# Optimization experiments

Measured on AMD Instinct MI355X. Metric: run time of the kernel, lower is better.

Reference implementation:

```python
import jax, jax.numpy as jnp
import numpy as np

N_NODES = 100000
N_EDGES = 1600000
NFEAT = 256
NHID = 64
NHEADS = 8
NCLASS = 97
ALPHA = 0.2  # leaky relu slope
EPS = 1e-16  # guard against isolated rows (pyGAT divides by e_rowsum directly)


def _sp_gat_layer(x, Wk, ak, src, dst, n_nodes, alpha, concat):
    """One SpGraphAttentionLayer (eval mode, dropout off).
    x: [N, f_in], Wk: [f_in, f_out], ak: [2*f_out].
    edge e_ij = exp(-leakyrelu(a . [h_i || h_j])), out[i] = sum_j e_ij h_j / sum_j e_ij.
    """
    h = x @ Wk                          # [N, f_out]
    f_out = Wk.shape[1]
    s_src = h @ ak[:f_out]              # [N] = a1 . h_i
    s_dst = h @ ak[f_out:]              # [N] = a2 . h_j
    e = jnp.exp(-jax.nn.leaky_relu(s_src[src] + s_dst[dst], negative_slope=alpha))  # [E]
    rowsum = jax.ops.segment_sum(e, src, num_segments=n_nodes)                       # [N]
    num = jax.ops.segment_sum(e[:, None] * h[dst], src, num_segments=n_nodes)        # [N, f_out]
    h_prime = num / (rowsum[:, None] + EPS)
    return jax.nn.elu(h_prime) if concat else h_prime


def setup_inputs() -> dict:
    key = jax.random.key(0)
    ks = jax.random.split(key, 6)
    gain = 1.414  # xavier gain used by pyGAT
    features = jax.random.normal(ks[0], (N_NODES, NFEAT), dtype=jnp.float32)
    edge_index = jax.random.randint(ks[1], (2, N_EDGES), 0, N_NODES, dtype=jnp.int64)
    W = jax.random.normal(ks[2], (NHEADS, NFEAT, NHID), dtype=jnp.float32) * (gain * np.sqrt(2.0 / (NFEAT + NHID)))
    a = jax.random.normal(ks[3], (NHEADS, 2 * NHID), dtype=jnp.float32) * (gain * np.sqrt(2.0 / (1 + 2 * NHID)))
    W_out = jax.random.normal(ks[4], (NHEADS * NHID, NCLASS), dtype=jnp.float32) * (gain * np.sqrt(2.0 / (NHEADS * NHID + NCLASS)))
    a_out = jax.random.normal(ks[5], (2 * NCLASS,), dtype=jnp.float32) * (gain * np.sqrt(2.0 / (1 + 2 * NCLASS)))
    return {"features": features, "W": W, "a": a, "W_out": W_out, "a_out": a_out, "edge_index": edge_index}


def reference(features, W, a, W_out, a_out, edge_index):
    src, dst = edge_index[0], edge_index[1]
    n = features.shape[0]
    # multi-head hidden layer, concat heads (loop over small fixed head count to bound memory)
    heads = [
        _sp_gat_layer(features, W[k], a[k], src, dst, n, ALPHA, concat=True)
        for k in range(W.shape[0])
    ]
    x = jnp.concatenate(heads, axis=1)  # [N, nheads*nhid]
    # output attention layer (concat=False), then elu + log_softmax as in SpGAT.forward
    x = _sp_gat_layer(x, W_out, a_out, src, dst, n, ALPHA, concat=False)
    return jax.nn.log_softmax(jax.nn.elu(x), axis=1)
```

## Files before the change

kernel.cpp:

```cpp
#include <hip/hip_runtime.h>
#include <hip/hip_bf16.h>
#include <stdint.h>

typedef __attribute__((ext_vector_type(8))) short short8;
typedef __attribute__((ext_vector_type(4))) float floatx4;
typedef uint32_t u32;

#define N_NODES 100000
#define N_EDGES 1600000
#define ALPHA_SLOPE 0.2f
#define EPS_F 1e-16f

static __device__ __forceinline__ float bf2f(ushort h) {
    u32 u = ((u32)h) << 16;
    return __builtin_bit_cast(float, u);
}
static __device__ __forceinline__ ushort f2bf(float f) {
    u32 u = __builtin_bit_cast(u32, f);
    u32 r = (u + 0x7fffu + ((u >> 16) & 1u)) >> 16;
    return (ushort)r;
}
static __device__ __forceinline__ float edge_e(float s) {
    float lr = s > 0.f ? s : ALPHA_SLOPE * s;
    return __expf(-lr);
}

__global__ __launch_bounds__(256) void prep(
    const float* __restrict__ feat, const float* __restrict__ W,
    const float* __restrict__ Wout, const float* __restrict__ a,
    const float* __restrict__ aout, const int* __restrict__ ei,
    ushort* __restrict__ featb, ushort* __restrict__ Bp1, ushort* __restrict__ Bp2,
    float* __restrict__ acol1, float* __restrict__ acol2, int* __restrict__ cnt)
{
    int b = blockIdx.x;
    if (b < 25000) {
        int i = b * 256 + threadIdx.x;
        float4 v = ((const float4*)feat)[i];
        ushort4 o;
        o.x = f2bf(v.x); o.y = f2bf(v.y); o.z = f2bf(v.z); o.w = f2bf(v.w);
        ((ushort4*)featb)[i] = o;
    } else if (b < 25512) {
        int idx = (b - 25000) * 256 + threadIdx.x;
        if (idx < 256 * 512) {
            int k = idx >> 9, n = idx & 511;
            int head = n >> 6, c = n & 63;
            Bp1[((size_t)(k >> 3) * 512 + n) * 8 + (k & 7)] = f2bf(W[head * 16384 + k * 64 + c]);
        }
        if (idx < 512 * 128) {
            int k = idx >> 7, n = idx & 127;
            ushort v = (n < 97) ? f2bf(Wout[k * 97 + n]) : (ushort)0;
            Bp2[((size_t)(k >> 3) * 128 + n) * 8 + (k & 7)] = v;
        }
        if (idx < 512) {
            int head = idx >> 6, c = idx & 63;
            acol1[idx * 2]     = a[head * 128 + c];
            acol1[idx * 2 + 1] = a[head * 128 + 64 + c];
        }
        if (idx < 128) {
            acol2[idx * 2]     = (idx < 97) ? aout[idx] : 0.f;
            acol2[idx * 2 + 1] = (idx < 97) ? aout[97 + idx] : 0.f;
        }
    } else {
        int e = (b - 25512) * 256 + threadIdx.x;
        atomicAdd(&cnt[ei[e]], 1);
    }
}

__global__ __launch_bounds__(256) void gemm_mfma(
    const ushort* __restrict__ A, const ushort* __restrict__ Bp,
    ushort* __restrict__ C, const float* __restrict__ acol,
    float* __restrict__ ssrc_arr, float* __restrict__ sdst_arr,
    int sstride, int M, int K, int NP)
{
    __shared__ __align__(16) ushort Ald[8 * 128 * 8];
    const int tid = threadIdx.x;
    const int lane = tid & 63;
    const int wave = tid >> 6;
    const int wr = wave >> 1, wc = wave & 1;
    const int row0 = blockIdx.y * 128;
    const int col0 = blockIdx.x * 128;
    const int quad = lane >> 4;
    const int l16 = lane & 15;

    floatx4 acc[4][4] = {};

    for (int k0 = 0; k0 < K; k0 += 64) {
        __syncthreads();
#pragma unroll
        for (int i = 0; i < 4; ++i) {
            int q = i * 256 + tid;
            int r = q >> 3, kq = q & 7;
            int row = row0 + r;
            if (row >= M) row = M - 1;
            const uint4* src = (const uint4*)(A + (size_t)row * K + k0 + kq * 8);
            *(uint4*)(&Ald[(kq * 128 + (r ^ kq)) * 8]) = *src;
        }
        __syncthreads();

#pragma unroll
        for (int s = 0; s < 2; ++s) {
            int kqq = s * 4 + quad;
            int kqg = (k0 >> 3) + kqq;
            short8 bfrag[4];
#pragma unroll
            for (int nt = 0; nt < 4; ++nt) {
                int col = col0 + wc * 64 + nt * 16 + l16;
                bfrag[nt] = *(const short8*)(Bp + ((size_t)kqg * NP + col) * 8);
            }
#pragma unroll
            for (int mt = 0; mt < 4; ++mt) {
                int r = wr * 64 + mt * 16 + l16;
                short8 afrag = *(const short8*)(&Ald[(kqq * 128 + (r ^ kqq)) * 8]);
#pragma unroll
                for (int nt = 0; nt < 4; ++nt) {
                    acc[mt][nt] = __builtin_amdgcn_mfma_f32_16x16x32_bf16(afrag, bfrag[nt], acc[mt][nt], 0, 0, 0);
                }
            }
        }
    }

#pragma unroll
    for (int mt = 0; mt < 4; ++mt) {
#pragma unroll
        for (int rr = 0; rr < 4; ++rr) {
            int row = row0 + wr * 64 + mt * 16 + quad * 4 + rr;
            if (row < M) {
#pragma unroll
                for (int nt = 0; nt < 4; ++nt) {
                    int col = col0 + wc * 64 + nt * 16 + l16;
                    C[(size_t)row * NP + col] = f2bf(acc[mt][nt][rr]);
                }
            }
        }
    }

    float av1[4], av2[4];
#pragma unroll
    for (int nt = 0; nt < 4; ++nt) {
        int col = col0 + wc * 64 + nt * 16 + l16;
        av1[nt] = acol[col * 2];
        av2[nt] = acol[col * 2 + 1];
    }
    int g = (col0 + wc * 64) >> 6;
    int goff = (sstride > 1) ? g : 0;
#pragma unroll
    for (int mt = 0; mt < 4; ++mt) {
#pragma unroll
        for (int rr = 0; rr < 4; ++rr) {
            float p1 = 0.f, p2 = 0.f;
#pragma unroll
            for (int nt = 0; nt < 4; ++nt) {
                p1 = fmaf(acc[mt][nt][rr], av1[nt], p1);
                p2 = fmaf(acc[mt][nt][rr], av2[nt], p2);
            }
#pragma unroll
            for (int o = 1; o < 16; o <<= 1) {
                p1 += __shfl_xor(p1, o);
                p2 += __shfl_xor(p2, o);
            }
            int row = row0 + wr * 64 + mt * 16 + quad * 4 + rr;
            if (l16 == 0 && row < M) {
                atomicAdd(&ssrc_arr[(size_t)row * sstride + goff], p1);
                atomicAdd(&sdst_arr[(size_t)row * sstride + goff], p2);
            }
        }
    }
}

__global__ __launch_bounds__(256) void scan_partial(const int* __restrict__ cnt, int* __restrict__ bsum, int N) {
    int idx = blockIdx.x * 256 + threadIdx.x;
    int v = (idx < N) ? cnt[idx] : 0;
#pragma unroll
    for (int o = 32; o; o >>= 1) v += __shfl_xor(v, o);
    __shared__ int ws[4];
    if ((threadIdx.x & 63) == 0) ws[threadIdx.x >> 6] = v;
    __syncthreads();
    if (threadIdx.x == 0) bsum[blockIdx.x] = ws[0] + ws[1] + ws[2] + ws[3];
}

__global__ __launch_bounds__(512) void scan_block(int* __restrict__ bsum, int nb) {
    __shared__ int s[512];
    int t = threadIdx.x;
    int v = (t < nb) ? bsum[t] : 0;
    s[t] = v;
    __syncthreads();
    for (int o = 1; o < 512; o <<= 1) {
        int u = (t >= o) ? s[t - o] : 0;
        __syncthreads();
        s[t] += u;
        __syncthreads();
    }
    if (t < nb) bsum[t] = s[t] - v;
}

__global__ __launch_bounds__(256) void scan_final(
    const int* __restrict__ cnt, const int* __restrict__ bsum,
    int* __restrict__ row_ptr, int N, int E)
{
    int b = blockIdx.x, t = threadIdx.x;
    int idx = b * 256 + t;
    int v = (idx < N) ? cnt[idx] : 0;
    __shared__ int s[256];
    s[t] = v;
    __syncthreads();
    for (int o = 1; o < 256; o <<= 1) {
        int u = (t >= o) ? s[t - o] : 0;
        __syncthreads();
        s[t] += u;
        __syncthreads();
    }
    if (idx < N) row_ptr[idx] = bsum[b] + s[t] - v;
    if (idx == 0) row_ptr[N] = E;
}

__global__ __launch_bounds__(256) void fill_csr(
    const int* __restrict__ ei, const int* __restrict__ row_ptr,
    int* __restrict__ cur, int* __restrict__ col_idx, int E)
{
    int e = blockIdx.x * 256 + threadIdx.x;
    if (e >= E) return;
    int s = ei[e];
    int d = ei[E + e];
    int p = atomicAdd(&cur[s], 1);
    col_idx[row_ptr[s] + p] = d;
}

__global__ __launch_bounds__(256) void ea1(
    const int* __restrict__ row_ptr, const int* __restrict__ col_idx,
    const ushort* __restrict__ h_all, const float* __restrict__ ssrc1,
    const float* __restrict__ sdst1, ushort* __restrict__ x1)
{
    int w = blockIdx.x * 4 + (threadIdx.x >> 6);
    int l = threadIdx.x & 63;
    int hl = l >> 3;
    int start = row_ptr[w], end = row_ptr[w + 1];
    float si = ssrc1[(size_t)w * 8 + hl];
    float acc[8] = {};
    float re = 0.f;
    int j = start;
    for (; j + 4 <= end; j += 4) {
        int d0 = col_idx[j], d1 = col_idx[j + 1], d2 = col_idx[j + 2], d3 = col_idx[j + 3];
        float e0 = edge_e(si + sdst1[(size_t)d0 * 8 + hl]);
        float e1 = edge_e(si + sdst1[(size_t)d1 * 8 + hl]);
        float e2 = edge_e(si + sdst1[(size_t)d2 * 8 + hl]);
        float e3 = edge_e(si + sdst1[(size_t)d3 * 8 + hl]);
        short8 v0 = *(const short8*)(h_all + (size_t)d0 * 512 + l * 8);
        short8 v1 = *(const short8*)(h_all + (size_t)d1 * 512 + l * 8);
        short8 v2 = *(const short8*)(h_all + (size_t)d2 * 512 + l * 8);
        short8 v3 = *(const short8*)(h_all + (size_t)d3 * 512 + l * 8);
        re += (e0 + e1) + (e2 + e3);
#pragma unroll
        for (int q = 0; q < 8; ++q) {
            float t0 = fmaf(e0, bf2f((ushort)v0[q]), e1 * bf2f((ushort)v1[q]));
            float t1 = fmaf(e2, bf2f((ushort)v2[q]), e3 * bf2f((ushort)v3[q]));
            acc[q] += t0 + t1;
        }
    }
    for (; j < end; ++j) {
        int d = col_idx[j];
        float e = edge_e(si + sdst1[(size_t)d * 8 + hl]);
        short8 hv = *(const short8*)(h_all + (size_t)d * 512 + l * 8);
        re += e;
#pragma unroll
        for (int q = 0; q < 8; ++q)
            acc[q] = fmaf(e, bf2f((ushort)hv[q]), acc[q]);
    }
    float inv = 1.f / (re + EPS_F);
    short8 o;
#pragma unroll
    for (int q = 0; q < 8; ++q) {
        float p = acc[q] * inv;
        p = p > 0.f ? p : expm1f(p);
        o[q] = (short)f2bf(p);
    }
    __builtin_nontemporal_store(o, (short8*)(x1 + (size_t)w * 512 + l * 8));
}

__global__ __launch_bounds__(256) void ea2(
    const int* __restrict__ row_ptr, const int* __restrict__ col_idx,
    const ushort* __restrict__ h2p, const float* __restrict__ s2src,
    const float* __restrict__ s2dst, float* __restrict__ out)
{
    int w = blockIdx.x * 8 + (threadIdx.x >> 5);
    int l = threadIdx.x & 31;
    int start = row_ptr[w], end = row_ptr[w + 1];
    float si = s2src[w];
    float a0 = 0.f, a1 = 0.f, a2 = 0.f, a3 = 0.f, re = 0.f;
    int j = start;
    for (; j + 4 <= end; j += 4) {
        int d0 = col_idx[j], d1 = col_idx[j + 1], d2 = col_idx[j + 2], d3 = col_idx[j + 3];
        float e0 = edge_e(si + s2dst[d0]);
        float e1 = edge_e(si + s2dst[d1]);
        float e2 = edge_e(si + s2dst[d2]);
        float e3 = edge_e(si + s2dst[d3]);
        ushort4 h0 = *(const ushort4*)(h2p + (size_t)d0 * 128 + 4 * l);
        ushort4 h1 = *(const ushort4*)(h2p + (size_t)d1 * 128 + 4 * l);
        ushort4 h2 = *(const ushort4*)(h2p + (size_t)d2 * 128 + 4 * l);
        ushort4 h3 = *(const ushort4*)(h2p + (size_t)d3 * 128 + 4 * l);
        re += (e0 + e1) + (e2 + e3);
        a0 += fmaf(e0, bf2f(h0.x), e1 * bf2f(h1.x)) + fmaf(e2, bf2f(h2.x), e3 * bf2f(h3.x));
        a1 += fmaf(e0, bf2f(h0.y), e1 * bf2f(h1.y)) + fmaf(e2, bf2f(h2.y), e3 * bf2f(h3.y));
        a2 += fmaf(e0, bf2f(h0.z), e1 * bf2f(h1.z)) + fmaf(e2, bf2f(h2.z), e3 * bf2f(h3.z));
        a3 += fmaf(e0, bf2f(h0.w), e1 * bf2f(h1.w)) + fmaf(e2, bf2f(h2.w), e3 * bf2f(h3.w));
    }
    for (; j < end; ++j) {
        int d = col_idx[j];
        float e = edge_e(si + s2dst[d]);
        ushort4 hv = *(const ushort4*)(h2p + (size_t)d * 128 + 4 * l);
        re += e;
        a0 = fmaf(e, bf2f(hv.x), a0);
        a1 = fmaf(e, bf2f(hv.y), a1);
        a2 = fmaf(e, bf2f(hv.z), a2);
        a3 = fmaf(e, bf2f(hv.w), a3);
    }
    float inv = 1.f / (re + EPS_F);
    float v[4] = { a0 * inv, a1 * inv, a2 * inv, a3 * inv };
    bool val[4];
    float m = -1e30f;
#pragma unroll
    for (int q = 0; q < 4; ++q) {
        v[q] = v[q] > 0.f ? v[q] : expm1f(v[q]);
        val[q] = (4 * l + q) < 97;
        if (val[q]) m = fmaxf(m, v[q]);
    }
#pragma unroll
    for (int o = 16; o; o >>= 1) m = fmaxf(m, __shfl_xor(m, o));
    float ex = 0.f;
#pragma unroll
    for (int q = 0; q < 4; ++q) ex += val[q] ? __expf(v[q] - m) : 0.f;
#pragma unroll
    for (int o = 16; o; o >>= 1) ex += __shfl_xor(ex, o);
    float lt = m + logf(ex);
#pragma unroll
    for (int q = 0; q < 4; ++q)
        if (val[q]) __builtin_nontemporal_store(v[q] - lt, out + (size_t)w * 97 + 4 * l + q);
}

extern "C" void kernel_launch(void* const* d_in, const int* in_sizes, int n_in,
                              void* d_out, int out_size, void* d_ws, size_t ws_size,
                              hipStream_t stream)
{
    const float* feat = (const float*)d_in[0];
    const float* W    = (const float*)d_in[1];
    const float* a    = (const float*)d_in[2];
    const float* Wout = (const float*)d_in[3];
    const float* aout = (const float*)d_in[4];
    const int*   ei   = (const int*)d_in[5];
    float* out = (float*)d_out;

    const int N = N_NODES, E = N_EDGES;
    const int NB = (N + 255) / 256;

    char* base = (char*)d_ws;
    ushort* h_all = (ushort*)(base);
    ushort* x1    = (ushort*)(base + 102400000);
    ushort* featb = (ushort*)(base + 204800000);
    ushort* h2p   = (ushort*)(base + 204800000);
    char* tail = base + 256000000;
    float* ssrc1   = (float*)(tail + 0);
    float* sdst1   = (float*)(tail + 3200000);
    float* s2src   = (float*)(tail + 6400000);
    float* s2dst   = (float*)(tail + 6800000);
    int*   row_ptr = (int*)(tail + 7200000);
    int*   cnt     = (int*)(tail + 7600128);
    int*   cur     = (int*)(tail + 8000128);
    int*   col_idx = (int*)(tail + 8400128);
    int*   bsum    = (int*)(tail + 14800128);
    ushort* Bp1    = (ushort*)(tail + 14801920);
    ushort* Bp2    = (ushort*)(tail + 15064064);
    float* acol1   = (float*)(tail + 15195136);
    float* acol2   = (float*)(tail + 15199232);

    hipMemsetAsync(ssrc1, 0, (size_t)8400128, stream);

    prep<<<31762, 256, 0, stream>>>(feat, W, Wout, a, aout, ei, featb, Bp1, Bp2, acol1, acol2, cnt);

    gemm_mfma<<<dim3(4, 782), 256, 0, stream>>>(featb, Bp1, h_all, acol1, ssrc1, sdst1, 8, N, 256, 512);

    scan_partial<<<NB, 256, 0, stream>>>(cnt, bsum, N);
    scan_block<<<1, 512, 0, stream>>>(bsum, NB);
    scan_final<<<NB, 256, 0, stream>>>(cnt, bsum, row_ptr, N, E);
    fill_csr<<<(E + 255) / 256, 256, 0, stream>>>(ei, row_ptr, cur, col_idx, E);

    ea1<<<N / 4, 256, 0, stream>>>(row_ptr, col_idx, h_all, ssrc1, sdst1, x1);

    gemm_mfma<<<dim3(1, 782), 256, 0, stream>>>(x1, Bp2, h2p, acol2, s2src, s2dst, 1, N, 512, 128);
    ea2<<<N / 8, 256, 0, stream>>>(row_ptr, col_idx, h2p, s2src, s2dst, out);
}
```

Baseline: 823.2 us.

## Fuse layer-1 attention aggregation with layer-2 projection GEMM via LDS tile

After: 774.5 us. 5.9% less time.

```diff
diff --git a/kernel.cpp b/kernel.cpp
--- a/kernel.cpp
+++ b/kernel.cpp
@@ -225,55 +225,112 @@
     col_idx[row_ptr[s] + p] = d;
 }
 
-__global__ __launch_bounds__(256) void ea1(
+__global__ __launch_bounds__(256, 6) void ea1p(
     const int* __restrict__ row_ptr, const int* __restrict__ col_idx,
     const ushort* __restrict__ h_all, const float* __restrict__ ssrc1,
-    const float* __restrict__ sdst1, ushort* __restrict__ x1)
-{
-    int w = blockIdx.x * 4 + (threadIdx.x >> 6);
-    int l = threadIdx.x & 63;
-    int hl = l >> 3;
-    int start = row_ptr[w], end = row_ptr[w + 1];
-    float si = ssrc1[(size_t)w * 8 + hl];
-    float acc[8] = {};
-    float re = 0.f;
-    int j = start;
-    for (; j + 4 <= end; j += 4) {
-        int d0 = col_idx[j], d1 = col_idx[j + 1], d2 = col_idx[j + 2], d3 = col_idx[j + 3];
-        float e0 = edge_e(si + sdst1[(size_t)d0 * 8 + hl]);
-        float e1 = edge_e(si + sdst1[(size_t)d1 * 8 + hl]);
-        float e2 = edge_e(si + sdst1[(size_t)d2 * 8 + hl]);
-        float e3 = edge_e(si + sdst1[(size_t)d3 * 8 + hl]);
-        short8 v0 = *(const short8*)(h_all + (size_t)d0 * 512 + l * 8);
-        short8 v1 = *(const short8*)(h_all + (size_t)d1 * 512 + l * 8);
-        short8 v2 = *(const short8*)(h_all + (size_t)d2 * 512 + l * 8);
-        short8 v3 = *(const short8*)(h_all + (size_t)d3 * 512 + l * 8);
-        re += (e0 + e1) + (e2 + e3);
+    const float* __restrict__ sdst1, const ushort* __restrict__ Bp2,
+    const float* __restrict__ acol2, ushort* __restrict__ h2p,
+    float* __restrict__ s2src, float* __restrict__ s2dst)
+{
+    __shared__ __align__(16) ushort Xs[16 * 512];
+    const int tid = threadIdx.x;
+    const int l = tid & 63;
+    const int wv = tid >> 6;
+    const int hl = l >> 3;
+    const int blk = blockIdx.x;
+
+#pragma unroll 1
+    for (int i = 0; i < 4; ++i) {
+        int r = wv * 4 + i;
+        int node = __builtin_amdgcn_readfirstlane(blk * 16 + r);
+        int start = row_ptr[node], end = row_ptr[node + 1];
+        float si = ssrc1[(size_t)node * 8 + hl];
+        float acc[8] = {};
+        float re = 0.f;
+        int j = start;
+        for (; j + 4 <= end; j += 4) {
+            int d0 = col_idx[j], d1 = col_idx[j + 1], d2 = col_idx[j + 2], d3 = col_idx[j + 3];
+            float e0 = edge_e(si + sdst1[(size_t)d0 * 8 + hl]);
+            float e1 = edge_e(si + sdst1[(size_t)d1 * 8 + hl]);
+            float e2 = edge_e(si + sdst1[(size_t)d2 * 8 + hl]);
+            float e3 = edge_e(si + sdst1[(size_t)d3 * 8 + hl]);
+            short8 v0 = *(const short8*)(h_all + (size_t)d0 * 512 + l * 8);
+            short8 v1 = *(const short8*)(h_all + (size_t)d1 * 512 + l * 8);
+            short8 v2 = *(const short8*)(h_all + (size_t)d2 * 512 + l * 8);
+            short8 v3 = *(const short8*)(h_all + (size_t)d3 * 512 + l * 8);
+            re += (e0 + e1) + (e2 + e3);
+#pragma unroll
+            for (int q = 0; q < 8; ++q) {
+                float t0 = fmaf(e0, bf2f((ushort)v0[q]), e1 * bf2f((ushort)v1[q]));
+                float t1 = fmaf(e2, bf2f((ushort)v2[q]), e3 * bf2f((ushort)v3[q]));
+                acc[q] += t0 + t1;
+            }
+        }
+        for (; j < end; ++j) {
+            int d = col_idx[j];
+            float e = edge_e(si + sdst1[(size_t)d * 8 + hl]);
+            short8 hv = *(const short8*)(h_all + (size_t)d * 512 + l * 8);
+            re += e;
+#pragma unroll
+            for (int q = 0; q < 8; ++q)
+                acc[q] = fmaf(e, bf2f((ushort)hv[q]), acc[q]);
+        }
+        float inv = 1.f / (re + EPS_F);
+        short8 o;
 #pragma unroll
         for (int q = 0; q < 8; ++q) {
-            float t0 = fmaf(e0, bf2f((ushort)v0[q]), e1 * bf2f((ushort)v1[q]));
-            float t1 = fmaf(e2, bf2f((ushort)v2[q]), e3 * bf2f((ushort)v3[q]));
-            acc[q] += t0 + t1;
-        }
-    }
-    for (; j < end; ++j) {
-        int d = col_idx[j];
-        float e = edge_e(si + sdst1[(size_t)d * 8 + hl]);
-        short8 hv = *(const short8*)(h_all + (size_t)d * 512 + l * 8);
-        re += e;
-#pragma unroll
-        for (int q = 0; q < 8; ++q)
-            acc[q] = fmaf(e, bf2f((ushort)hv[q]), acc[q]);
-    }
-    float inv = 1.f / (re + EPS_F);
-    short8 o;
-#pragma unroll
-    for (int q = 0; q < 8; ++q) {
-        float p = acc[q] * inv;
-        p = p > 0.f ? p : expm1f(p);
-        o[q] = (short)f2bf(p);
-    }
-    __builtin_nontemporal_store(o, (short8*)(x1 + (size_t)w * 512 + l * 8));
+            float p = acc[q] * inv;
+            p = p > 0.f ? p : expm1f(p);
+            o[q] = (short)f2bf(p);
+        }
+        *(short8*)(&Xs[((size_t)r * 64 + (size_t)(l ^ (r & 7))) * 8]) = o;
+    }
+    __syncthreads();
+
+    const int l16 = l & 15;
+    const int g = l >> 4;
+    floatx4 acc2[2] = {};
+#pragma unroll
+    for (int s = 0; s < 16; ++s) {
+        int c = s * 4 + g;
+        short8 afrag = *(const short8*)(&Xs[((size_t)l16 * 64 + (size_t)(c ^ (l16 & 7))) * 8]);
+#pragma unroll
+        for (int nt = 0; nt < 2; ++nt) {
+            int col = wv * 32 + nt * 16 + l16;
+            short8 bfrag = *(const short8*)(Bp2 + ((size_t)c * 128 + col) * 8);
+            acc2[nt] = __builtin_amdgcn_mfma_f32_16x16x32_bf16(afrag, bfrag, acc2[nt], 0, 0, 0);
+        }
+    }
+
+    float av1[2], av2[2];
+#pragma unroll
+    for (int nt = 0; nt < 2; ++nt) {
+        int col = wv * 32 + nt * 16 + l16;
+        av1[nt] = acol2[col * 2];
+        av2[nt] = acol2[col * 2 + 1];
+    }
+#pragma unroll
+    for (int rr = 0; rr < 4; ++rr) {
+        int row = g * 4 + rr;
+        int node = blk * 16 + row;
+        float p1 = 0.f, p2 = 0.f;
+#pragma unroll
+        for (int nt = 0; nt < 2; ++nt) {
+            int col = wv * 32 + nt * 16 + l16;
+            h2p[(size_t)node * 128 + col] = f2bf(acc2[nt][rr]);
+            p1 = fmaf(acc2[nt][rr], av1[nt], p1);
+            p2 = fmaf(acc2[nt][rr], av2[nt], p2);
+        }
+#pragma unroll
+        for (int o = 1; o < 16; o <<= 1) {
+            p1 += __shfl_xor(p1, o);
+            p2 += __shfl_xor(p2, o);
+        }
+        if (l16 == 0) {
+            atomicAdd(&s2src[node], p1);
+            atomicAdd(&s2dst[node], p2);
+        }
+    }
 }
 
 __global__ __launch_bounds__(256) void ea2(
@@ -353,7 +410,6 @@
 
     char* base = (char*)d_ws;
     ushort* h_all = (ushort*)(base);
-    ushort* x1    = (ushort*)(base + 102400000);
     ushort* featb = (ushort*)(base + 204800000);
     ushort* h2p   = (ushort*)(base + 204800000);
     char* tail = base + 256000000;
@@ -382,8 +438,7 @@
     scan_final<<<NB, 256, 0, stream>>>(cnt, bsum, row_ptr, N, E);
     fill_csr<<<(E + 255) / 256, 256, 0, stream>>>(ei, row_ptr, cur, col_idx, E);
 
-    ea1<<<N / 4, 256, 0, stream>>>(row_ptr, col_idx, h_all, ssrc1, sdst1, x1);
-
-    gemm_mfma<<<dim3(1, 782), 256, 0, stream>>>(x1, Bp2, h2p, acol2, s2src, s2dst, 1, N, 512, 128);
+    ea1p<<<N / 16, 256, 0, stream>>>(row_ptr, col_idx, h_all, ssrc1, sdst1, Bp2, acol2, h2p, s2src, s2dst);
+
     ea2<<<N / 8, 256, 0, stream>>>(row_ptr, col_idx, h2p, s2src, s2dst, out);
 }
```
